# Kernel optimization log

Measured on AMD Instinct MI355X. Metric: run time of the kernel, lower is better.

The kernel has to match this reference:

```python
import jax, jax.numpy as jnp
import numpy as np

WAY = 5
TEMPERATURE = 0.2
TEMPERATURE_ATTN = 5.0
BN_EPS = 1e-5


def bn_apply(x, p):
    # p: (4, C) = gamma, beta, running_mean, running_var (eval-mode BatchNorm)
    g, b, m, v = p[0], p[1], p[2], p[3]
    sh = (1, -1) + (1,) * (x.ndim - 2)
    return (x - m.reshape(sh)) * (g.reshape(sh) / jnp.sqrt(v.reshape(sh) + BN_EPS)) + b.reshape(sh)


def conv3d(x, w, pad):
    return jax.lax.conv_general_dilated(
        x, w, (1, 1, 1), [(pad[0], pad[0]), (pad[1], pad[1]), (pad[2], pad[2])],
        dimension_numbers=('NCDHW', 'OIDHW', 'NCDHW'))


def sepconv4d(x, conv2_w, bn2, conv1_w, bn1, proj_w, bnp):
    # x: (b, c, u, v, h, w). conv2: (k,k,1) kernel over (u,v); conv1: (1,k,k) over (h,w).
    b, c, u, v, h, w = x.shape
    y = x.reshape(b, c, u, v, h * w)
    y = bn_apply(conv3d(y, conv2_w, (1, 1, 0)), bn2)
    y = jax.nn.relu(y)
    y = y.reshape(b, c, u * v, h, w)
    y = bn_apply(conv3d(y, conv1_w, (0, 1, 1)), bn1)
    # 1x1 projection (pointwise over channels) + BN
    y = jnp.einsum('oc,bcxhw->boxhw', proj_w, y)
    y = bn_apply(y, bnp)
    return y.reshape(b, -1, u, v, h, w)


def cca(x, c1, c2):
    def branch(z):
        z = sepconv4d(z, *c1)
        z = jax.nn.relu(z)
        z = sepconv4d(z, *c2)
        return z
    perm = (0, 1, 4, 5, 2, 3)
    return branch(x) + jnp.transpose(branch(jnp.transpose(x, perm)), perm)


def gaussian_normalize(x, axis, eps=1e-5):
    m = jnp.mean(x, axis=axis, keepdims=True)
    v = jnp.var(x, axis=axis, keepdims=True, ddof=1)  # torch.var is unbiased
    return (x - m) / jnp.sqrt(v + eps)


def setup_inputs() -> dict:
    key = jax.random.key(0)
    ks = jax.random.split(key, 16)

    def bn_params(k, c):
        k1, k2, k3, k4 = jax.random.split(k, 4)
        g = 1.0 + 0.1 * jax.random.normal(k1, (c,), jnp.float32)
        b = 0.1 * jax.random.normal(k2, (c,), jnp.float32)
        m = 0.1 * jax.random.normal(k3, (c,), jnp.float32)
        v = 1.0 + 0.1 * jax.random.uniform(k4, (c,), jnp.float32)
        return jnp.stack([g, b, m, v])

    return {
        'spt': jax.random.normal(ks[0], (1, 5, 640, 10, 10), jnp.float32),
        'qry': jax.random.normal(ks[1], (75, 640, 10, 10), jnp.float32),
        'w_1x1': jax.random.normal(ks[2], (64, 640), jnp.float32) * 0.04,
        'bn_1x1': bn_params(ks[3], 64),
        'c1_conv2_w': jax.random.normal(ks[4], (1, 1, 3, 3, 1), jnp.float32) * 0.33,
        'c1_bn2': bn_params(ks[5], 1),
        'c1_conv1_w': jax.random.normal(ks[6], (1, 1, 1, 3, 3), jnp.float32) * 0.33,
        'c1_bn1': bn_params(ks[7], 1),
        'c1_proj_w': jax.random.normal(ks[8], (16, 1), jnp.float32),
        'c1_bnp': bn_params(ks[9], 16),
        'c2_conv2_w': jax.random.normal(ks[10], (16, 16, 3, 3, 1), jnp.float32) * 0.083,
        'c2_bn2': bn_params(ks[11], 16),
        'c2_conv1_w': jax.random.normal(ks[12], (16, 16, 1, 3, 3), jnp.float32) * 0.083,
        'c2_bn1': bn_params(ks[13], 16),
        'c2_proj_w': jax.random.normal(ks[14], (1, 16), jnp.float32) * 0.25,
        'c2_bnp': bn_params(ks[15], 1),
    }


def reference(spt, qry, w_1x1, bn_1x1,
              c1_conv2_w, c1_bn2, c1_conv1_w, c1_bn1, c1_proj_w, c1_bnp,
              c2_conv2_w, c2_bn2, c2_conv1_w, c2_bn1, c2_proj_w, c2_bnp):
    s = spt[0]                                   # (way, C, H, W)
    s = s - s.mean(axis=1, keepdims=True)        # normalize_feature
    q = qry - qry.mean(axis=1, keepdims=True)

    def cca1x1(x):
        y = jnp.einsum('oc,bchw->bohw', w_1x1, x)
        return jax.nn.relu(bn_apply(y, bn_1x1))

    sf = cca1x1(s)
    qf = cca1x1(q)
    sf = sf / jnp.maximum(jnp.linalg.norm(sf, axis=1, keepdims=True), 1e-8)
    qf = qf / jnp.maximum(jnp.linalg.norm(qf, axis=1, keepdims=True), 1e-8)

    # 4D correlation (avoids the repeat-induced 6D blowup of the original)
    corr = jnp.einsum('ncij,qckl->qnijkl', sf, qf)  # (Q, way, Hs, Ws, Hq, Wq)
    Q, way, Hs, Ws, Hq, Wq = corr.shape

    c1 = (c1_conv2_w, c1_bn2, c1_conv1_w, c1_bn1, c1_proj_w, c1_bnp)
    c2 = (c2_conv2_w, c2_bn2, c2_conv1_w, c2_bn1, c2_proj_w, c2_bnp)
    corr = cca(corr.reshape(Q * way, 1, Hs, Ws, Hq, Wq), c1, c2)

    corr_s = corr.reshape(Q, way, Hs * Ws, Hq, Wq)
    corr_q = corr.reshape(Q, way, Hs, Ws, Hq * Wq)
    corr_s = gaussian_normalize(corr_s, axis=2)
    corr_q = gaussian_normalize(corr_q, axis=4)
    corr_s = jax.nn.softmax(corr_s / TEMPERATURE_ATTN, axis=2).reshape(Q, way, Hs, Ws, Hq, Wq)
    corr_q = jax.nn.softmax(corr_q / TEMPERATURE_ATTN, axis=4).reshape(Q, way, Hs, Ws, Hq, Wq)

    attn_s = corr_s.sum(axis=(4, 5))             # (Q, way, Hs, Ws)
    attn_q = corr_q.sum(axis=(2, 3))             # (Q, way, Hq, Wq)

    spt_att = (attn_s[:, :, None] * s[None]).mean(axis=(-1, -2))       # (Q, way, C)
    qry_att = (attn_q[:, :, None] * q[:, None]).mean(axis=(-1, -2))    # (Q, way, C)
    qry_pooled = q.mean(axis=(-1, -2))                                  # (Q, C)

    num = jnp.sum(spt_att * qry_att, axis=-1)
    den = (jnp.maximum(jnp.linalg.norm(spt_att, axis=-1), 1e-8) *
           jnp.maximum(jnp.linalg.norm(qry_att, axis=-1), 1e-8))
    sim = (num / den) / TEMPERATURE
    return sim, qry_pooled
```

## Files before the change

kernel.cpp:

```cpp
#include <hip/hip_runtime.h>


#define NITEM 375

#define OFF_XTS 0
#define OFF_XTQ 160000
#define OFF_MP  2560000
#define OFF_SF  2568000
#define OFF_QF  2600000
#define OFF_RA  3080000
#define OFF_RB  6830000
#define OFF_PRM 10655000

#define PK2F 232
#define PK1F 1512
#define WSUMF 2792
#define SCVF 2856
#define SHVF 2920
#define PKWF 2984

#define Y1REG    20480
#define Y1HSTR4  17600
#define Y1SSTR4  35200
#define Y1INT    22080
#define ZPB4     20480
#define Y2S4     129280
#define Y2HH     16128
#define LDS_TOTAL4 161536

typedef float f4v __attribute__((ext_vector_type(4)));
typedef float f32x4 __attribute__((ext_vector_type(4)));
typedef _Float16 half8v __attribute__((ext_vector_type(8)));
typedef __fp16 fp16x2 __attribute__((ext_vector_type(2)));
typedef unsigned int u32x4 __attribute__((ext_vector_type(4)));
typedef unsigned int u32x2 __attribute__((ext_vector_type(2)));

__device__ __forceinline__ unsigned int pkrtz(float a, float b) {
  union { fp16x2 h; unsigned int u; } cv;
  cv.h = __builtin_amdgcn_cvt_pkrtz(a, b);
  return cv.u;
}

__global__ __launch_bounds__(256) void k_prep(
    const float* __restrict__ w1x1,  const float* __restrict__ bn1x1,
    const float* __restrict__ c1c2w, const float* __restrict__ c1bn2,
    const float* __restrict__ c1c1w, const float* __restrict__ c1bn1,
    const float* __restrict__ c1pj,  const float* __restrict__ c1bnp,
    const float* __restrict__ c2c2w, const float* __restrict__ c2bn2,
    const float* __restrict__ c2c1w, const float* __restrict__ c2bn1,
    const float* __restrict__ c2pj,  const float* __restrict__ c2bnp,
    float* __restrict__ prm)
{
  const int t = threadIdx.x;
  const float eps = 1e-5f;

  if (blockIdx.x < 64) {
    __shared__ float red[4];
    _Float16* pkw = (_Float16*)(prm + PKWF);
    const int base = blockIdx.x * 800;
    for (int r = t; r < 800; r += 256) {
      int idx = base + r;
      int fi = idx >> 9, rem = idx & 511;
      int ln = rem >> 3, j = rem & 7;
      int cc = fi / 10, r2 = fi - cc * 10;
      int mt = r2 >> 1, kk = r2 & 1;
      int m = mt * 16 + (ln & 15);
      int k = cc * 64 + kk * 32 + ((ln >> 4) & 3) * 8 + j;
      float v = (m < 64) ? w1x1[m * 640 + k] : (m == 64 ? 1.f : 0.f);
      pkw[idx] = (_Float16)v;
    }
    const int o = blockIdx.x;
    float s = 0.f;
    for (int c = t; c < 640; c += 256) s += w1x1[o * 640 + c];
    #pragma unroll
    for (int off = 32; off > 0; off >>= 1) s += __shfl_down(s, off);
    if ((t & 63) == 0) red[t >> 6] = s;
    __syncthreads();
    if (t == 0) {
      prm[WSUMF + o] = red[0] + red[1] + red[2] + red[3];
      float scv = bn1x1[o] / sqrtf(bn1x1[192 + o] + eps);
      prm[SCVF + o] = scv;
      prm[SHVF + o] = bn1x1[64 + o] - bn1x1[128 + o] * scv;
    }
    return;
  }

  for (int idx = t; idx < 144; idx += 256) {
    int ds = idx / 16, i = idx % 16;
    float spv = c2bnp[0] / sqrtf(c2bnp[3] + eps);
    float acc = 0.f;
    for (int o = 0; o < 16; ++o) {
      float s1 = c2bn1[o] / sqrtf(c2bn1[48 + o] + eps);
      acc += c2pj[o] * s1 * c2c1w[(o * 16 + i) * 9 + ds];
    }
    prm[idx] = spv * acc;
  }
  for (int i = t; i < 16; i += 256) {
    float s = c1bnp[i] / sqrtf(c1bnp[48 + i] + eps);
    prm[144 + i] = s * c1pj[i];
    prm[160 + i] = c1bnp[16 + i] - c1bnp[32 + i] * s;
  }
  for (int o = t; o < 16; o += 256) {
    float s = c2bn2[o] / sqrtf(c2bn2[48 + o] + eps);
    prm[176 + o] = s;
    prm[192 + o] = c2bn2[16 + o] - c2bn2[32 + o] * s;
  }
  for (int k = t; k < 9; k += 256) {
    prm[208 + k] = c1c2w[k];
    prm[217 + k] = c1c1w[k];
  }
  if (t == 0) {
    float S2 = c1bn2[0] / sqrtf(c1bn2[3] + eps);
    prm[226] = S2;
    prm[227] = c1bn2[1] - c1bn2[2] * S2;
    float S1 = c1bn1[0] / sqrtf(c1bn1[3] + eps);
    prm[228] = S1;
    prm[229] = c1bn1[1] - c1bn1[2] * S1;
    float spv = c2bnp[0] / sqrtf(c2bnp[3] + eps);
    float k0 = 0.f;
    for (int o = 0; o < 16; ++o) {
      float s1 = c2bn1[o] / sqrtf(c2bn1[48 + o] + eps);
      k0 += c2pj[o] * (c2bn1[16 + o] - c2bn1[32 + o] * s1);
    }
    prm[230] = spv * (k0 - c2bnp[2]) + c2bnp[1];
    prm[231] = 0.f;
  }
  __syncthreads();

  _Float16* pk2 = (_Float16*)(prm + PK2F);
  for (int idx = t; idx < 2560; idx += 256) {
    int c = idx >> 9, rem = idx & 511;
    int ln = rem >> 3, j = rem & 7;
    int o = ln & 15, qq = ln >> 4;
    int tap = 2 * c + (qq >> 1);
    int i = (qq & 1) * 8 + j;
    float v = (tap < 9) ? c2c2w[(o * 16 + i) * 9 + tap] : 0.f;
    pk2[idx] = (_Float16)v;
  }
  _Float16* pk1 = (_Float16*)(prm + PK1F);
  for (int idx = t; idx < 2560; idx += 256) {
    int c = idx >> 9, rem = idx & 511;
    int ln = rem >> 3, j = rem & 7;
    int m = ln & 15, qq = ln >> 4;
    int k = c * 32 + qq * 8 + j;
    int tp = k >> 4, i = k & 15;
    float v = (m == 0 && tp < 9) ? prm[tp * 16 + i] : 0.f;
    pk1[idx] = (_Float16)v;
  }
}

__global__ __launch_bounds__(512) void k_feat(
    const float* __restrict__ spt, const float* __restrict__ qry,
    float* __restrict__ ws, float* __restrict__ out)
{
  __shared__ __align__(16) char POOL[2 * 16128];
  __shared__ __align__(16) float mrow[112];
  __shared__ __align__(16) float rn[112];
  __shared__ float CS[2][512];
  __shared__ float RS[640];
  __shared__ float msumL;

  const int b = blockIdx.x, t = threadIdx.x;
  const int lane = t & 63, wvv = t >> 6;
  const int n0 = lane & 15, qd = (lane >> 4) & 3;
  const float* src = (b < 5) ? spt + b * 64000 : qry + (b - 5) * 64000;
  unsigned int* xtg = (unsigned int*)(ws + ((b < 5) ? (OFF_XTS + b * 32000)
                                                    : (OFF_XTQ + (b - 5) * 32000)));
  const float* prm = ws + OFF_PRM;
  const _Float16* pkw = (const _Float16*)(prm + PKWF);

  for (int idx = t; idx < 864; idx += 512) {
    int bsel = idx / 432, r = idx - bsel * 432;
    ((unsigned int*)(POOL + bsel * 16128 + 100 * 144))[r] = 0u;
  }
  for (int u = t; u < 800; u += 512) {
    int cp = u / 25, p4 = u - cp * 25;
    const float* r0 = src + (2 * cp) * 100 + p4 * 4;
    f4v a = *(const f4v*)r0;
    f4v c1 = *(const f4v*)(r0 + 100);
    #pragma unroll
    for (int e = 0; e < 4; ++e)
      *(unsigned int*)((_Float16*)POOL + (p4 * 4 + e) * 72 + 2 * cp) = pkrtz(a[e], c1[e]);
  }
  __syncthreads();

  const int chp = t >> 3, part = t & 7;
  const int pLo = part * 13, pHi = (pLo + 13 < 100) ? pLo + 13 : 100;

  f32x4 acc[5];
  #pragma unroll
  for (int ti = 0; ti < 5; ++ti) { acc[ti][0]=0.f; acc[ti][1]=0.f; acc[ti][2]=0.f; acc[ti][3]=0.f; }

  for (int cc = 0; cc < 10; ++cc) {
    const int cur = cc & 1;
    const _Float16* Xc = (const _Float16*)(POOL + cur * 16128);
    _Float16* Xn = (_Float16*)(POOL + (cur ^ 1) * 16128);

    f4v pa[2], pc[2];
    if (cc < 9) {
      #pragma unroll
      for (int k = 0; k < 2; ++k) {
        int u = t + k * 512;
        if (u < 800) {
          int cp = u / 25, p4 = u - cp * 25;
          const float* r0 = src + ((cc + 1) * 64 + 2 * cp) * 100 + p4 * 4;
          pa[k] = *(const f4v*)r0;
          pc[k] = *(const f4v*)(r0 + 100);
        }
      }
    }
    for (int u = t; u < 3200; u += 512) {
      int p = u >> 5, cp = u & 31;
      xtg[p * 320 + cc * 32 + cp] = *(const unsigned int*)(Xc + p * 72 + 2 * cp);
    }
    #pragma unroll
    for (int kk = 0; kk < 2; ++kk) {
      #pragma unroll
      for (int ti = 0; ti < 5; ++ti) {
        int idx = wvv + ti * 8; if (idx > 34) idx = 34;
        int mt = idx / 7, nt = idx - mt * 7;
        half8v av = *(const half8v*)(pkw + (cc * 10 + mt * 2 + kk) * 512 + lane * 8);
        half8v bv = *(const half8v*)(Xc + (nt * 16 + n0) * 72 + kk * 32 + qd * 8);
        acc[ti] = __builtin_amdgcn_mfma_f32_16x16x32_f16(av, bv, acc[ti], 0, 0, 0);
      }
    }
    {
      float s = 0.f;
      for (int p = pLo; p < pHi; ++p) s += (float)Xc[p * 72 + chp];
      CS[cur][t] = s;
    }
    if (cc < 9) {
      #pragma unroll
      for (int k = 0; k < 2; ++k) {
        int u = t + k * 512;
        if (u < 800) {
          int cp = u / 25, p4 = u - cp * 25;
          #pragma unroll
          for (int e = 0; e < 4; ++e)
            *(unsigned int*)(Xn + (p4 * 4 + e) * 72 + 2 * cp) = pkrtz(pa[k][e], pc[k][e]);
        }
      }
    }
    __syncthreads();
    if (t < 64) {
      float s = 0.f;
      #pragma unroll
      for (int k = 0; k < 8; ++k) s += CS[cur][t * 8 + k];
      RS[cc * 64 + t] = s;
    }
  }
  #pragma unroll
  for (int ti = 0; ti < 5; ++ti) {
    int idx = wvv + ti * 8; if (idx > 34) idx = 34;
    int mt = idx / 7, nt = idx - mt * 7;
    if (mt == 4 && qd == 0) {
      int p = nt * 16 + n0;
      mrow[p] = acc[ti][0] * (1.f / 640.f);
    }
  }
  __syncthreads();
  float* OUT = (float*)POOL;
  if (t == 0) { float s = 0.f; for (int p = 0; p < 100; ++p) s += mrow[p]; msumL = s; }
  #pragma unroll
  for (int ti = 0; ti < 5; ++ti) {
    int idx = wvv + ti * 8; if (idx > 34) idx = 34;
    int mt = idx / 7, nt = idx - mt * 7;
    if (mt < 4) {
      int p = nt * 16 + n0;
      if (p < 100) {
        float mp = mrow[p];
        #pragma unroll
        for (int r = 0; r < 4; ++r) {
          int o = mt * 16 + qd * 4 + r;
          float v = acc[ti][r] - prm[WSUMF + o] * mp;
          v = prm[SCVF + o] * v + prm[SHVF + o];
          OUT[o * 104 + p] = v > 0.f ? v : 0.f;
        }
      }
    }
  }
  __syncthreads();
  if (t < 100) {
    float s = 0.f;
    for (int o = 0; o < 64; ++o) { float v = OUT[o * 104 + t]; s += v * v; }
    float nr = sqrtf(s);
    rn[t] = 1.f / (nr > 1e-8f ? nr : 1e-8f);
    ws[OFF_MP + b * 100 + t] = mrow[t];
  }
  __syncthreads();
  {
    unsigned int* fg = (unsigned int*)((b < 5) ? (ws + OFF_SF) : (ws + OFF_QF))
                       + ((b < 5) ? b : (b - 5)) * 3584;
    for (int idx = t; idx < 3584; idx += 512) {
      const int jj = idx & 3;
      const int ln2 = (idx >> 2) & 63;
      const int fi = idx >> 8;
      const int kk = fi / 7, pt = fi - kk * 7;
      const int pos = pt * 16 + (ln2 & 15);
      const int c0 = kk * 32 + ((ln2 >> 4) & 3) * 8 + 2 * jj;
      float a = 0.f, bb = 0.f;
      if (pos < 100) {
        const float rv = rn[pos];
        a = OUT[c0 * 104 + pos] * rv;
        bb = OUT[(c0 + 1) * 104 + pos] * rv;
      }
      fg[idx] = pkrtz(a, bb);
    }
  }
  if (b >= 5) {
    const float msum = msumL;
    for (int gc = t; gc < 640; gc += 512)
      out[375 + (b - 5) * 640 + gc] = (RS[gc] - msum) * 0.01f;
  }
}

__global__ __launch_bounds__(1024) __attribute__((amdgpu_waves_per_eu(4, 4)))
void k_cca(float* __restrict__ ws)
{
  extern __shared__ char smem[];
  _Float16* T2h = (_Float16*)smem;
  float* T1   = (float*)(smem + 20480);
  float* CORR = (float*)(smem + 84480);

  const float* prm = ws + OFF_PRM;
  const int bid = blockIdx.x;
  const int it = bid >> 1, br = bid & 1;
  const int q = it / 5, n = it % 5;
  const int t = threadIdx.x;
  const int lane = t & 63, wv = t >> 6;
  const int n0 = lane & 15, qd = (lane >> 4) & 3;
  const int qh = qd >> 1, ih = qd & 1;

  const _Float16* pk2 = (const _Float16*)(prm + PK2F);
  const _Float16* pk1 = (const _Float16*)(prm + PK1F);
  half8v A2[5], A1[5];
  #pragma unroll
  for (int c = 0; c < 5; ++c) {
    A2[c] = *(const half8v*)(pk2 + c * 512 + lane * 8);
    A1[c] = *(const half8v*)(pk1 + c * 512 + lane * 8);
  }
  float sc2[4], bc2[4];
  #pragma unroll
  for (int r = 0; r < 4; ++r) { sc2[r] = prm[176 + qd * 4 + r]; bc2[r] = prm[192 + qd * 4 + r]; }

  const int d1E[5] = {-1,-1, 0, 0, 1}, d2E[5] = {-1, 1, 0,-1, 1};
  const int d1O[5] = {-1, 0, 0, 1, 0}, d2O[5] = { 0,-1, 1, 0, 0};

  int pp1[4], st1[4], addr2[4][5], posB[4];
  bool pv[4];
  #pragma unroll
  for (int ti = 0; ti < 4; ++ti) {
    int tile = wv + ti * 16; if (tile > 62) tile = 62;
    const int p = tile * 16 + n0;
    const int pcp = p < 1000 ? p : 999;
    pp1[ti] = pcp * 16;
    st1[ti] = Y2S4 + qh * Y2HH + p * 16 + ih * 8;
    pv[ti] = (qd == 0) && (p < 1000);
    const int f2 = pcp / 100;
    const int s = pcp - f2 * 100;
    const int s1 = s / 10, s2 = s - s1 * 10;
    const bool rm = s1 > 0, rp = s1 < 9, cm = s2 > 0, cp2 = s2 < 9;
    const int b0 = Y2S4 + ih * Y2HH + pcp * 16;
    #pragma unroll
    for (int c = 0; c < 5; ++c) {
      const bool vE = (d1E[c] < 0 ? rm : (d1E[c] > 0 ? rp : true)) &&
                      (d2E[c] < 0 ? cm : (d2E[c] > 0 ? cp2 : true));
      const bool vO = (c == 4) ? false :
                      ((d1O[c] < 0 ? rm : (d1O[c] > 0 ? rp : true)) &&
                       (d2O[c] < 0 ? cm : (d2O[c] > 0 ? cp2 : true)));
      const bool v = qh ? vO : vE;
      const int D1c = (qh ? (d1O[c] * 10 + d2O[c]) : (d1E[c] * 10 + d2E[c]));
      addr2[ti][c] = v ? (b0 + D1c * 16) : ZPB4;
    }
    posB[ti] = br ? (s * 100 + f2) : (f2 * 100 + s);
  }
  const int posStride = br ? 10 : 1000;

  {
    const half8v* fS = (const half8v*)(ws + OFF_SF) + n * 896;
    const half8v* fQ = (const half8v*)(ws + OFF_QF) + q * 896;
    const half8v* FA = br ? fQ : fS;
    const half8v* FB = br ? fS : fQ;
    #pragma unroll
    for (int ti = 0; ti < 4; ++ti) {
      int T = wv + ti * 16; if (T > 48) T = 48;
      const int mt = T / 7, nt = T - mt * 7;
      half8v a0 = FA[mt * 64 + lane];
      half8v b0 = FB[nt * 64 + lane];
      half8v a1 = FA[(7 + mt) * 64 + lane];
      half8v b1 = FB[(7 + nt) * 64 + lane];
      f32x4 acc; acc[0]=0.f; acc[1]=0.f; acc[2]=0.f; acc[3]=0.f;
      acc = __builtin_amdgcn_mfma_f32_16x16x32_f16(a0, b0, acc, 0, 0, 0);
      acc = __builtin_amdgcn_mfma_f32_16x16x32_f16(a1, b1, acc, 0, 0, 0);
      const int s = nt * 16 + n0;
      if (s < 100) {
        const int s1a = s / 10;
        float* cp0 = CORR + s1a * 16 + (s - s1a * 10);
        const int r0 = mt * 16 + qd * 4;
        #pragma unroll
        for (int r = 0; r < 4; ++r)
          if (r0 + r < 100) cp0[(r0 + r) * 160] = acc[r];
      }
    }
  }
  __syncthreads();

  const float S2 = prm[226], B2 = prm[227], S1 = prm[228], B1 = prm[229];

  if (t < 600) {
    const int h = t / 300, r2 = t - h * 300;
    const int f2 = r2 / 30, r3 = r2 - f2 * 30;
    const int s1v = r3 / 3, s2q = r3 - s1v * 3;
    const int cb = s1v * 16 + s2q * 4;
    f4v outv[5];
    #pragma unroll
    for (int i = 0; i < 5; ++i) { outv[i][0]=0.f; outv[i][1]=0.f; outv[i][2]=0.f; outv[i][3]=0.f; }
    #pragma unroll
    for (int k = 0; k < 7; ++k) {
      const int nf1 = 5 * h - 1 + k;
      if ((unsigned)nf1 >= 10u) continue;
      #pragma unroll
      for (int dv = 0; dv < 3; ++dv) {
        const int nf2 = f2 + dv - 1;
        if ((unsigned)nf2 >= 10u) continue;
        f4v x = *(const f4v*)(CORR + (nf1 * 10 + nf2) * 160 + cb);
        #pragma unroll
        for (int du = 0; du < 3; ++du) {
          const int f1l = k - du;
          if (f1l < 0 || f1l > 4) continue;
          const float w = prm[208 + du * 3 + dv];
          #pragma unroll
          for (int e = 0; e < 4; ++e) outv[f1l][e] += w * x[e];
        }
      }
    }
    #pragma unroll
    for (int f1l = 0; f1l < 5; ++f1l) {
      const int f = (5 * h + f1l) * 10 + f2;
      f4v v;
      #pragma unroll
      for (int e = 0; e < 4; ++e) { float z = S2 * outv[f1l][e] + B2; v[e] = z > 0.f ? z : 0.f; }
      *(f4v*)(T1 + f * 160 + cb) = v;
    }
  }
  __syncthreads();

  if (t < 1000) {
    const int f = t / 10, s1 = t - (t / 10) * 10;
    const float* rowB = T1 + f * 160;
    f4v r[3][3];
    float w[3][3];
    #pragma unroll
    for (int dh = 0; dh < 3; ++dh) {
      int rr = s1 + dh - 1;
      bool okr = (unsigned)rr < 10u;
      int rc = rr < 0 ? 0 : (rr > 9 ? 9 : rr);
      const float* rp = rowB + rc * 16;
      r[dh][0] = *(const f4v*)(rp);
      r[dh][1] = *(const f4v*)(rp + 4);
      r[dh][2] = *(const f4v*)(rp + 8);
      #pragma unroll
      for (int dw = 0; dw < 3; ++dw) w[dh][dw] = okr ? prm[217 + dh * 3 + dw] : 0.f;
    }
    float o[10];
    #pragma unroll
    for (int s2 = 0; s2 < 10; ++s2) {
      float a = 0.f;
      #pragma unroll
      for (int dh = 0; dh < 3; ++dh)
        #pragma unroll
        for (int dw = 0; dw < 3; ++dw) {
          int col = s2 + dw - 1;
          if (col < 0 || col > 9) continue;
          a += w[dh][dw] * r[dh][col >> 2][col & 3];
        }
      o[s2] = a;
    }
    unsigned int* dst = (unsigned int*)((char*)T2h + (f * 100 + s1 * 10) * 2);
    #pragma unroll
    for (int k = 0; k < 5; ++k)
      dst[k] = pkrtz(S1 * o[2 * k] + B1, S1 * o[2 * k + 1] + B1);
  }
  __syncthreads();

  #define GEN_Y1(F1N)                                                          \
    if (t < 1000) {                                                            \
      const int _sl = (F1N) % 3;                                               \
      const float t2 = (float)T2h[(F1N) * 1000 + t];                           \
      unsigned int d[8];                                                       \
      _Pragma("unroll")                                                        \
      for (int j = 0; j < 8; ++j) {                                            \
        float ya = fmaxf(prm[144 + 2 * j] * t2 + prm[160 + 2 * j], 0.f);       \
        float yb = fmaxf(prm[145 + 2 * j] * t2 + prm[161 + 2 * j], 0.f);       \
        d[j] = pkrtz(ya, yb);                                                  \
      }                                                                        \
      u32x4 lo, hi;                                                            \
      lo[0]=d[0]; lo[1]=d[1]; lo[2]=d[2]; lo[3]=d[3];                          \
      hi[0]=d[4]; hi[1]=d[5]; hi[2]=d[6]; hi[3]=d[7];                          \
      *(u32x4*)(smem + Y1INT + _sl * Y1SSTR4 + t * 16) = lo;                   \
      *(u32x4*)(smem + Y1INT + _sl * Y1SSTR4 + Y1HSTR4 + t * 16) = hi;         \
    }

  GEN_Y1(0)
  GEN_Y1(1)
  {
    u32x4 zz; zz[0] = 0u; zz[1] = 0u; zz[2] = 0u; zz[3] = 0u;
    for (int idx = t; idx < 700; idx += 1024) {
      const int r = idx / 100;
      *(u32x4*)(smem + Y1REG + r * Y1HSTR4 + (idx - r * 100) * 16) = zz;
    }
    for (int idx = t; idx < 2000; idx += 1024) {
      const int h = idx >= 1000 ? 1 : 0;
      *(u32x4*)(smem + Y1INT + 2 * Y1SSTR4 + h * Y1HSTR4 + (idx - h * 1000) * 16) = zz;
    }
  }
  __syncthreads();

  const float Cf = prm[230];
  float* resb = ws + (br ? OFF_RB : OFF_RA) + it * 10000;
  int gp = 0;

  for (int g = 0; g < 10; ++g) {
    const int o0 = (g % 3) * Y1SSTR4;
    const int oP = ((g + 1) % 3) * Y1SSTR4;
    const int oM = ((g + 2) % 3) * Y1SSTR4;
    int base1[5];
    #pragma unroll
    for (int c = 0; c < 5; ++c) {
      const int eb = (d1E[c] < 0 ? oM : (d1E[c] > 0 ? oP : o0)) + d2E[c] * 1600;
      const int ob = (d1O[c] < 0 ? oM : (d1O[c] > 0 ? oP : o0)) + d2O[c] * 1600;
      base1[c] = Y1INT + ih * Y1HSTR4 + (qh ? ob : eb);
    }

    #pragma unroll
    for (int ti = 0; ti < 4; ++ti) {
      f32x4 acc; acc[0]=0.f; acc[1]=0.f; acc[2]=0.f; acc[3]=0.f;
      #pragma unroll
      for (int c = 0; c < 5; ++c) {
        half8v b = *(const half8v*)(smem + base1[c] + pp1[ti]);
        acc = __builtin_amdgcn_mfma_f32_16x16x32_f16(A2[c], b, acc, 0, 0, 0);
      }
      const float v0 = fmaxf(sc2[0] * acc[0] + bc2[0], 0.f);
      const float v1 = fmaxf(sc2[1] * acc[1] + bc2[1], 0.f);
      const float v2 = fmaxf(sc2[2] * acc[2] + bc2[2], 0.f);
      const float v3 = fmaxf(sc2[3] * acc[3] + bc2[3], 0.f);
      u32x2 wq; wq[0] = pkrtz(v0, v1); wq[1] = pkrtz(v2, v3);
      *(u32x2*)(smem + st1[ti]) = wq;
    }
    __syncthreads();

    #pragma unroll
    for (int ti = 0; ti < 4; ++ti) {
      f32x4 acc; acc[0]=0.f; acc[1]=0.f; acc[2]=0.f; acc[3]=0.f;
      #pragma unroll
      for (int c = 0; c < 5; ++c) {
        half8v b = *(const half8v*)(smem + addr2[ti][c]);
        acc = __builtin_amdgcn_mfma_f32_16x16x32_f16(A1[c], b, acc, 0, 0, 0);
      }
      if (pv[ti]) resb[posB[ti] + gp] = acc[0] + Cf;
    }
    if (g + 2 <= 9) { GEN_Y1(g + 2) }
    else if (g == 8) {
      u32x4 zz; zz[0] = 0u; zz[1] = 0u; zz[2] = 0u; zz[3] = 0u;
      for (int idx = t; idx < 2000; idx += 1024) {
        const int h = idx >= 1000 ? 1 : 0;
        *(u32x4*)(smem + Y1INT + Y1SSTR4 + h * Y1HSTR4 + (idx - h * 1000) * 16) = zz;
      }
    }
    gp += posStride;
    __syncthreads();
  }
  #undef GEN_Y1
}

__global__ __launch_bounds__(256) void k_post(float* __restrict__ ws,
                                              float* __restrict__ out)
{
  __shared__ float F[10000];
  __shared__ float mc[100], ic[100], rc[100];
  __shared__ float mr[100], ir[100], rr[100];
  __shared__ float asL[100], aqL[100], msL[100], mqL[100];
  __shared__ float alph[2];
  __shared__ float red[12];
  const int it = blockIdx.x, t = threadIdx.x;
  const int q = it / 5, n = it % 5;

  const f4v* ra4 = (const f4v*)(ws + OFF_RA + it * 10000);
  const f4v* rb4 = (const f4v*)(ws + OFF_RB + it * 10000);
  f4v* F4 = (f4v*)F;
  for (int idx = t; idx < 2500; idx += 256) {
    f4v a = ra4[idx], b = rb4[idx];
    #pragma unroll
    for (int e = 0; e < 4; ++e) a[e] += b[e];
    F4[idx] = a;
  }
  if (t < 100) msL[t] = ws[OFF_MP + n * 100 + t];
  else if (t < 200) mqL[t - 100] = ws[OFF_MP + (5 + q) * 100 + t - 100];
  __syncthreads();

  if (t < 100) {
    float s = 0.f;
    for (int ij = 0; ij < 100; ++ij) s += F[ij * 100 + t];
    float m = s * 0.01f;
    float ss = 0.f;
    for (int ij = 0; ij < 100; ++ij) { float d = F[ij * 100 + t] - m; ss += d * d; }
    float inv = 1.f / (sqrtf(ss * (1.f / 99.f) + 1e-5f) * 5.f);
    float den = 0.f;
    for (int ij = 0; ij < 100; ++ij) den += __expf((F[ij * 100 + t] - m) * inv);
    mc[t] = m; ic[t] = inv; rc[t] = 1.f / den;
  } else if (t < 200) {
    const int r = t - 100;
    float s = 0.f;
    for (int kl = 0; kl < 100; ++kl) s += F[r * 100 + kl];
    float m = s * 0.01f;
    float ss = 0.f;
    for (int kl = 0; kl < 100; ++kl) { float d = F[r * 100 + kl] - m; ss += d * d; }
    float inv = 1.f / (sqrtf(ss * (1.f / 99.f) + 1e-5f) * 5.f);
    float den = 0.f;
    for (int kl = 0; kl < 100; ++kl) den += __expf((F[r * 100 + kl] - m) * inv);
    mr[r] = m; ir[r] = inv; rr[r] = 1.f / den;
  }
  __syncthreads();
  if (t < 100) {
    float s = 0.f;
    for (int kl = 0; kl < 100; ++kl)
      s += __expf((F[t * 100 + kl] - mc[kl]) * ic[kl]) * rc[kl];
    asL[t] = s;
  } else if (t < 200) {
    const int r = t - 100;
    float s2 = 0.f;
    for (int ij = 0; ij < 100; ++ij)
      s2 += __expf((F[ij * 100 + r] - mr[ij]) * ir[ij]) * rr[ij];
    aqL[r] = s2;
  }
  __syncthreads();
  if (t < 2) {
    float s = 0.f;
    for (int p = 0; p < 100; ++p) s += t ? (aqL[p] * mqL[p]) : (asL[p] * msL[p]);
    alph[t] = s;
  }
  __syncthreads();

  const unsigned int* xs = (const unsigned int*)(ws + OFF_XTS + n * 32000);
  const unsigned int* xq = (const unsigned int*)(ws + OFF_XTQ + q * 32000);
  const float als = alph[0], alq = alph[1];
  float dot = 0.f, na = 0.f, nb = 0.f;
  for (int u = t; u < 320; u += 256) {
    float s0 = 0.f, s1 = 0.f, q0 = 0.f, q1 = 0.f;
    for (int p = 0; p < 100; ++p) {
      union { unsigned int u; fp16x2 h; } a, bq;
      a.u = xs[p * 320 + u];
      bq.u = xq[p * 320 + u];
      float ap = asL[p], qp = aqL[p];
      s0 += ap * (float)a.h[0]; s1 += ap * (float)a.h[1];
      q0 += qp * (float)bq.h[0]; q1 += qp * (float)bq.h[1];
    }
    float sa0 = (s0 - als) * 0.01f, sa1 = (s1 - als) * 0.01f;
    float qa0 = (q0 - alq) * 0.01f, qa1 = (q1 - alq) * 0.01f;
    dot += sa0 * qa0 + sa1 * qa1;
    na  += sa0 * sa0 + sa1 * sa1;
    nb  += qa0 * qa0 + qa1 * qa1;
  }
  #pragma unroll
  for (int off = 32; off > 0; off >>= 1) {
    dot += __shfl_down(dot, off);
    na  += __shfl_down(na, off);
    nb  += __shfl_down(nb, off);
  }
  const int wid = t >> 6, lanei = t & 63;
  if (lanei == 0) { red[wid * 3 + 0] = dot; red[wid * 3 + 1] = na; red[wid * 3 + 2] = nb; }
  __syncthreads();
  if (t == 0) {
    dot = red[0] + red[3] + red[6] + red[9];
    na  = red[1] + red[4] + red[7] + red[10];
    nb  = red[2] + red[5] + red[8] + red[11];
    float ns = sqrtf(na); ns = ns > 1e-8f ? ns : 1e-8f;
    float nq2 = sqrtf(nb); nq2 = nq2 > 1e-8f ? nq2 : 1e-8f;
    out[it] = dot / (ns * nq2) * 5.f;
  }
}

extern "C" void kernel_launch(void* const* d_in, const int* in_sizes, int n_in,
                              void* d_out, int out_size, void* d_ws, size_t ws_size,
                              hipStream_t stream)
{
  (void)in_sizes; (void)n_in; (void)out_size; (void)ws_size;
  const float* spt    = (const float*)d_in[0];
  const float* qry    = (const float*)d_in[1];
  const float* w1x1   = (const float*)d_in[2];
  const float* bn1x1  = (const float*)d_in[3];
  const float* c1c2w  = (const float*)d_in[4];
  const float* c1bn2  = (const float*)d_in[5];
  const float* c1c1w  = (const float*)d_in[6];
  const float* c1bn1  = (const float*)d_in[7];
  const float* c1pj   = (const float*)d_in[8];
  const float* c1bnp  = (const float*)d_in[9];
  const float* c2c2w  = (const float*)d_in[10];
  const float* c2bn2  = (const float*)d_in[11];
  const float* c2c1w  = (const float*)d_in[12];
  const float* c2bn1  = (const float*)d_in[13];
  const float* c2pj   = (const float*)d_in[14];
  const float* c2bnp  = (const float*)d_in[15];
  float* ws  = (float*)d_ws;
  float* out = (float*)d_out;

  k_prep<<<65, 256, 0, stream>>>(w1x1, bn1x1,
                                 c1c2w, c1bn2, c1c1w, c1bn1, c1pj, c1bnp,
                                 c2c2w, c2bn2, c2c1w, c2bn1, c2pj, c2bnp,
                                 ws + OFF_PRM);
  k_feat<<<80, 512, 0, stream>>>(spt, qry, ws, out);

  (void)hipFuncSetAttribute((const void*)k_cca,
                            hipFuncAttributeMaxDynamicSharedMemorySize, LDS_TOTAL4);
  k_cca<<<NITEM * 2, 1024, LDS_TOTAL4, stream>>>(ws);

  k_post<<<NITEM, 256, 0, stream>>>(ws, out);
}
```

Before: 315.2 us.

## Fuse first pointwise projection into MFMA operand build instead of staging Y1 in LDS

Rather than expanding the 1-channel intermediate into a 16-channel fp16 Y1 ring buffer in shared memory each slice, the kernel now keeps the padded single-channel T2 plane in LDS. It recomputes the 8 ReLU(a*t+b) channel values per lane right before each MFMA. The padding is set to a NaN-like fp16 pattern so out-of-range taps presumably produce zeros after the ReLU. This removes the Y1 generation pass, its zeroing and the larger LDS footprint, at the cost of extra ALU work and scalar 2-byte LDS reads inside the MFMA loop.

```diff
diff --git a/kernel.cpp b/kernel.cpp
--- a/kernel.cpp
+++ b/kernel.cpp
@@ -19,14 +19,15 @@
 #define SHVF 2920
 #define PKWF 2984
 
-#define Y1REG    20480
-#define Y1HSTR4  17600
-#define Y1SSTR4  35200
-#define Y1INT    22080
-#define ZPB4     20480
-#define Y2S4     129280
+#define T2GAP    200
+#define T2SSTR   2200
+#define T2INT0   2400
+#define ZPB5     26608
+#define T1B      26688
+#define CORRB    90688
+#define Y2S5     26688
 #define Y2HH     16128
-#define LDS_TOTAL4 161536
+#define LDS_TOTAL5 154688
 
 typedef float f4v __attribute__((ext_vector_type(4)));
 typedef float f32x4 __attribute__((ext_vector_type(4)));
@@ -318,9 +319,8 @@
 void k_cca(float* __restrict__ ws)
 {
   extern __shared__ char smem[];
-  _Float16* T2h = (_Float16*)smem;
-  float* T1   = (float*)(smem + 20480);
-  float* CORR = (float*)(smem + 84480);
+  float* T1   = (float*)(smem + T1B);
+  float* CORR = (float*)(smem + CORRB);
 
   const float* prm = ws + OFF_PRM;
   const int bid = blockIdx.x;
@@ -343,24 +343,37 @@
   #pragma unroll
   for (int r = 0; r < 4; ++r) { sc2[r] = prm[176 + qd * 4 + r]; bc2[r] = prm[192 + qd * 4 + r]; }
 
+  float AvL[8], BpL[8];
+  #pragma unroll
+  for (int j = 0; j < 8; ++j) {
+    AvL[j] = prm[144 + ih * 8 + j];
+    BpL[j] = prm[160 + ih * 8 + j];
+  }
+
   const int d1E[5] = {-1,-1, 0, 0, 1}, d2E[5] = {-1, 1, 0,-1, 1};
   const int d1O[5] = {-1, 0, 0, 1, 0}, d2O[5] = { 0,-1, 1, 0, 0};
 
-  int pp1[4], st1[4], addr2[4][5], posB[4];
+  int pos2[4], st1[4], addr2[4][5], posB[4], D1F[5];
   bool pv[4];
+  #pragma unroll
+  for (int c = 0; c < 5; ++c) {
+    const int d1 = qh ? d1O[c] : d1E[c];
+    const int d2 = qh ? d2O[c] : d2E[c];
+    D1F[c] = d1 * T2SSTR + d2 * 200;
+  }
   #pragma unroll
   for (int ti = 0; ti < 4; ++ti) {
     int tile = wv + ti * 16; if (tile > 62) tile = 62;
     const int p = tile * 16 + n0;
     const int pcp = p < 1000 ? p : 999;
-    pp1[ti] = pcp * 16;
-    st1[ti] = Y2S4 + qh * Y2HH + p * 16 + ih * 8;
+    pos2[ti] = pcp * 2;
+    st1[ti] = Y2S5 + qh * Y2HH + p * 16 + ih * 8;
     pv[ti] = (qd == 0) && (p < 1000);
     const int f2 = pcp / 100;
     const int s = pcp - f2 * 100;
     const int s1 = s / 10, s2 = s - s1 * 10;
     const bool rm = s1 > 0, rp = s1 < 9, cm = s2 > 0, cp2 = s2 < 9;
-    const int b0 = Y2S4 + ih * Y2HH + pcp * 16;
+    const int b0 = Y2S5 + ih * Y2HH + pcp * 16;
     #pragma unroll
     for (int c = 0; c < 5; ++c) {
       const bool vE = (d1E[c] < 0 ? rm : (d1E[c] > 0 ? rp : true)) &&
@@ -370,7 +383,7 @@
                        (d2O[c] < 0 ? cm : (d2O[c] > 0 ? cp2 : true)));
       const bool v = qh ? vO : vE;
       const int D1c = (qh ? (d1O[c] * 10 + d2O[c]) : (d1E[c] * 10 + d2E[c]));
-      addr2[ti][c] = v ? (b0 + D1c * 16) : ZPB4;
+      addr2[ti][c] = v ? (b0 + D1c * 16) : ZPB5;
     }
     posB[ti] = br ? (s * 100 + f2) : (f2 * 100 + s);
   }
@@ -442,6 +455,16 @@
       for (int e = 0; e < 4; ++e) { float z = S2 * outv[f1l][e] + B2; v[e] = z > 0.f ? z : 0.f; }
       *(f4v*)(T1 + f * 160 + cb) = v;
     }
+  } else {
+    const unsigned NN = 0x7E007E00u;
+    for (int z = t - 600; z < 1650; z += 424) {
+      int addr;
+      if (z < 550) addr = z * 4;
+      else if (z < 1100) addr = 24400 + (z - 550) * 4;
+      else { int k = z - 1100; int gi = k / 50 + 1; addr = gi * T2SSTR + (k - (gi - 1) * 50) * 4; }
+      *(unsigned*)(smem + addr) = NN;
+    }
+    if (t - 600 < 4) *(unsigned*)(smem + ZPB5 + (t - 600) * 4) = 0u;
   }
   __syncthreads();
 
@@ -476,43 +499,11 @@
         }
       o[s2] = a;
     }
-    unsigned int* dst = (unsigned int*)((char*)T2h + (f * 100 + s1 * 10) * 2);
+    const int f1 = f / 10, f2 = f - f1 * 10;
+    unsigned int* dst = (unsigned int*)(smem + T2INT0 + f1 * T2SSTR + (f2 * 100 + s1 * 10) * 2);
     #pragma unroll
     for (int k = 0; k < 5; ++k)
       dst[k] = pkrtz(S1 * o[2 * k] + B1, S1 * o[2 * k + 1] + B1);
-  }
-  __syncthreads();
-
-  #define GEN_Y1(F1N)                                                          \
-    if (t < 1000) {                                                            \
-      const int _sl = (F1N) % 3;                                               \
-      const float t2 = (float)T2h[(F1N) * 1000 + t];                           \
-      unsigned int d[8];                                                       \
-      _Pragma("unroll")                                                        \
-      for (int j = 0; j < 8; ++j) {                                            \
-        float ya = fmaxf(prm[144 + 2 * j] * t2 + prm[160 + 2 * j], 0.f);       \
-        float yb = fmaxf(prm[145 + 2 * j] * t2 + prm[161 + 2 * j], 0.f);       \
-        d[j] = pkrtz(ya, yb);                                                  \
-      }                                                                        \
-      u32x4 lo, hi;                                                            \
-      lo[0]=d[0]; lo[1]=d[1]; lo[2]=d[2]; lo[3]=d[3];                          \
-      hi[0]=d[4]; hi[1]=d[5]; hi[2]=d[6]; hi[3]=d[7];                          \
-      *(u32x4*)(smem + Y1INT + _sl * Y1SSTR4 + t * 16) = lo;                   \
-      *(u32x4*)(smem + Y1INT + _sl * Y1SSTR4 + Y1HSTR4 + t * 16) = hi;         \
-    }
-
-  GEN_Y1(0)
-  GEN_Y1(1)
-  {
-    u32x4 zz; zz[0] = 0u; zz[1] = 0u; zz[2] = 0u; zz[3] = 0u;
-    for (int idx = t; idx < 700; idx += 1024) {
-      const int r = idx / 100;
-      *(u32x4*)(smem + Y1REG + r * Y1HSTR4 + (idx - r * 100) * 16) = zz;
-    }
-    for (int idx = t; idx < 2000; idx += 1024) {
-      const int h = idx >= 1000 ? 1 : 0;
-      *(u32x4*)(smem + Y1INT + 2 * Y1SSTR4 + h * Y1HSTR4 + (idx - h * 1000) * 16) = zz;
-    }
   }
   __syncthreads();
 
@@ -521,24 +512,21 @@
   int gp = 0;
 
   for (int g = 0; g < 10; ++g) {
-    const int o0 = (g % 3) * Y1SSTR4;
-    const int oP = ((g + 1) % 3) * Y1SSTR4;
-    const int oM = ((g + 2) % 3) * Y1SSTR4;
-    int base1[5];
-    #pragma unroll
-    for (int c = 0; c < 5; ++c) {
-      const int eb = (d1E[c] < 0 ? oM : (d1E[c] > 0 ? oP : o0)) + d2E[c] * 1600;
-      const int ob = (d1O[c] < 0 ? oM : (d1O[c] > 0 ? oP : o0)) + d2O[c] * 1600;
-      base1[c] = Y1INT + ih * Y1HSTR4 + (qh ? ob : eb);
-    }
+    const int gB = T2INT0 + g * T2SSTR;
 
     #pragma unroll
     for (int ti = 0; ti < 4; ++ti) {
       f32x4 acc; acc[0]=0.f; acc[1]=0.f; acc[2]=0.f; acc[3]=0.f;
       #pragma unroll
       for (int c = 0; c < 5; ++c) {
-        half8v b = *(const half8v*)(smem + base1[c] + pp1[ti]);
-        acc = __builtin_amdgcn_mfma_f32_16x16x32_f16(A2[c], b, acc, 0, 0, 0);
+        const int ad = gB + D1F[c] + pos2[ti];
+        const float t2f = (float)(*(const __fp16*)(smem + ad));
+        union { u32x4 u; half8v h; } bb;
+        #pragma unroll
+        for (int jj = 0; jj < 4; ++jj)
+          bb.u[jj] = pkrtz(fmaxf(AvL[2 * jj] * t2f + BpL[2 * jj], 0.f),
+                           fmaxf(AvL[2 * jj + 1] * t2f + BpL[2 * jj + 1], 0.f));
+        acc = __builtin_amdgcn_mfma_f32_16x16x32_f16(A2[c], bb.h, acc, 0, 0, 0);
       }
       const float v0 = fmaxf(sc2[0] * acc[0] + bc2[0], 0.f);
       const float v1 = fmaxf(sc2[1] * acc[1] + bc2[1], 0.f);
@@ -559,18 +547,9 @@
       }
       if (pv[ti]) resb[posB[ti] + gp] = acc[0] + Cf;
     }
-    if (g + 2 <= 9) { GEN_Y1(g + 2) }
-    else if (g == 8) {
-      u32x4 zz; zz[0] = 0u; zz[1] = 0u; zz[2] = 0u; zz[3] = 0u;
-      for (int idx = t; idx < 2000; idx += 1024) {
-        const int h = idx >= 1000 ? 1 : 0;
-        *(u32x4*)(smem + Y1INT + Y1SSTR4 + h * Y1HSTR4 + (idx - h * 1000) * 16) = zz;
-      }
-    }
     gp += posStride;
     __syncthreads();
   }
-  #undef GEN_Y1
 }
 
 __global__ __launch_bounds__(256) void k_post(float* __restrict__ ws,
@@ -711,8 +690,8 @@
   k_feat<<<80, 512, 0, stream>>>(spt, qry, ws, out);
 
   (void)hipFuncSetAttribute((const void*)k_cca,
-                            hipFuncAttributeMaxDynamicSharedMemorySize, LDS_TOTAL4);
-  k_cca<<<NITEM * 2, 1024, LDS_TOTAL4, stream>>>(ws);
+                            hipFuncAttributeMaxDynamicSharedMemorySize, LDS_TOTAL5);
+  k_cca<<<NITEM * 2, 1024, LDS_TOTAL5, stream>>>(ws);
 
   k_post<<<NITEM, 256, 0, stream>>>(ws, out);
 }
```

Result: slower. 341.1 us (+8.2%).
